# Optimization experiments

Hardware: AMD Instinct MI355X
Metric: run time of the kernel (lower is better)

Reference implementation:

```python
import jax, jax.numpy as jnp
import numpy as np

RADIUS = 50
HEADS = 4
BN_EPS = 1e-5


def setup_inputs() -> dict:
    key = jax.random.key(0)
    B, C, L = 2, 256, 1536
    D = C // HEADS
    ks = jax.random.split(key, 8)
    s = 0.05  # weight init scale
    return {
        "x": jax.random.normal(ks[0], (B, C, L), jnp.float32),
        "Wc": jax.random.normal(ks[1], (C, C), jnp.float32) * s,
        "bc": jnp.zeros((C,), jnp.float32),
        "Wq": jax.random.normal(ks[2], (C, C), jnp.float32) * s,
        "bq": jnp.zeros((C,), jnp.float32),
        "Wk": jax.random.normal(ks[3], (C, C), jnp.float32) * s,
        "bk": jnp.zeros((C,), jnp.float32),
        "emb": jax.random.normal(ks[4], (2 * RADIUS + 1, D), jnp.float32) * s,
        "Wf": jax.random.normal(ks[5], (C, C), jnp.float32) * s,
        "bf": jnp.zeros((C,), jnp.float32),
        "gamma": jnp.ones((C,), jnp.float32),
        "beta": jnp.zeros((C,), jnp.float32),
        "scale": jnp.full((C,), 0.1, jnp.float32),
    }


def reference(x, Wc, bc, Wq, bq, Wk, bk, emb, Wf, bf, gamma, beta, scale):
    B, C, L = x.shape
    H = HEADS
    D = C // H
    R = RADIUS

    def conv1x1(W, b, y):  # 1x1 Conv1d == per-position matmul
        return jnp.einsum('oc,bcl->bol', W, y) + b[None, :, None]

    def split(y):  # [B,C,L] -> [B,H,D,L]
        return y.reshape(B, H, D, L)

    content = split(conv1x1(Wc, bc, x))
    query = split(conv1x1(Wq, bq, x))
    key_ = split(conv1x1(Wk, bk, x))

    steps = jnp.arange(L)
    relative = steps[:, None] - steps[None, :]                 # [L,L]
    rel_clamped = jnp.clip(relative, -R, R)
    embs = emb[R + rel_clamped]                                # [L,L,D] gather

    dots = jnp.einsum('bhct,bhcs->bhts', query, key_)          # [B,H,L,L]
    dots = dots + 0.3 * jnp.einsum('bhct,tsc->bhts', query, embs)
    dots = jnp.where(jnp.abs(relative) <= R, dots, -jnp.inf)   # band mask

    weights = jax.nn.softmax(dots, axis=-1)                    # [B,H,L,L]

    out = jnp.einsum('bhts,bhcs->bhct', weights, content)      # [B,H,D,L]
    out = out + 0.3 * jnp.einsum('bhts,tsc->bhct', weights, embs)
    out = out.reshape(B, C, L)

    out = conv1x1(Wf, bf, out)
    # BatchNorm1d in training mode: batch stats over (B, L) per channel
    mean = out.mean(axis=(0, 2), keepdims=True)
    var = out.var(axis=(0, 2), keepdims=True)
    out = (out - mean) / jnp.sqrt(var + BN_EPS)
    out = out * gamma[None, :, None] + beta[None, :, None]
    return jax.nn.relu(out) * scale[None, :, None]
```

## Files before the change

### kernel.cpp

```cpp
#include <hip/hip_runtime.h>

typedef unsigned short u16;
typedef unsigned int u32;
typedef __bf16 bf16x8 __attribute__((ext_vector_type(8)));
typedef float f32x4 __attribute__((ext_vector_type(4)));

#define MFMA16 __builtin_amdgcn_mfma_f32_16x16x32_bf16

__device__ __forceinline__ u16 f2bf(float f) {
    u32 u = __float_as_uint(f);
    u32 r = (u + 0x7fffu + ((u >> 16) & 1u)) >> 16;
    return (u16)r;
}
__device__ __forceinline__ float bf2f(u16 h) {
    return __uint_as_float(((u32)h) << 16);
}
__device__ __forceinline__ bf16x8 ld8(const u16* p) {
    return *reinterpret_cast<const bf16x8*>(p);
}

__global__ __launch_bounds__(256) void prep_x(const float* __restrict__ x,
                                              u16* __restrict__ xT)
{
    __shared__ u16 tile[64][65];
    const int tid = threadIdx.x;
    const int b = blockIdx.z, c0 = blockIdx.y * 64, l0 = blockIdx.x * 64;
    const int cc = tid >> 2, lq = (tid & 3) * 16;
    const float* xp = x + (size_t)((b * 256 + c0 + cc) * 1536 + l0 + lq);
    #pragma unroll
    for (int i = 0; i < 4; ++i) {
        float4 v = *reinterpret_cast<const float4*>(xp + i * 4);
        tile[cc][lq + i * 4 + 0] = f2bf(v.x);
        tile[cc][lq + i * 4 + 1] = f2bf(v.y);
        tile[cc][lq + i * 4 + 2] = f2bf(v.z);
        tile[cc][lq + i * 4 + 3] = f2bf(v.w);
    }
    __syncthreads();
    const int ll = tid >> 2, cq = (tid & 3) * 16;
    u16* op = xT + (size_t)((b * 1536 + l0 + ll) * 256 + c0 + cq);
    #pragma unroll
    for (int i = 0; i < 16; ++i) op[i] = tile[cq + i][ll];
}

__global__ __launch_bounds__(256) void prep_we(
    const float* __restrict__ Wc, const float* __restrict__ Wq,
    const float* __restrict__ Wk, const float* __restrict__ Wf,
    const float* __restrict__ emb,
    u16* __restrict__ wcb, u16* __restrict__ wqb, u16* __restrict__ wkb,
    u16* __restrict__ wfb, u16* __restrict__ embR, u16* __restrict__ embT)
{
    const int i = blockIdx.x * 256 + threadIdx.x;
    if (i < 65536) {
        wcb[i] = f2bf(Wc[i]); wqb[i] = f2bf(Wq[i]);
        wkb[i] = f2bf(Wk[i]); wfb[i] = f2bf(Wf[i]);
    }
    if (i < 112 * 64) {
        int j = i >> 6, d = i & 63;
        embR[i] = (j < 101) ? f2bf(0.3f * emb[(100 - j) * 64 + d]) : (u16)0;
    }
    if (i < 64 * 128) {
        int d = i >> 7, j = i & 127;
        embT[i] = (j < 101) ? f2bf(0.3f * emb[(100 - j) * 64 + d]) : (u16)0;
    }
}

__global__ __launch_bounds__(256) void gemm_qk(
    const u16* __restrict__ xT,
    const u16* __restrict__ Wq, const float* __restrict__ bq,
    const u16* __restrict__ Wk, const float* __restrict__ bk,
    u16* __restrict__ qo, u16* __restrict__ ko)
{
    const int tid = threadIdx.x, wv = tid >> 6, lane = tid & 63;
    const int l15 = lane & 15, kg8 = (lane >> 4) * 8;
    const int z = blockIdx.z, b = z & 1, which = z >> 1;
    const u16* W = which ? Wk : Wq;
    const float* bias = which ? bk : bq;
    u16* outp = which ? ko : qo;
    const int m0 = blockIdx.x * 64 + (wv & 1) * 32;
    const int ch0 = blockIdx.y * 64 + (wv >> 1) * 32;
    const u16* ap = xT + (size_t)(b * 1536 + m0 + l15) * 256 + kg8;
    const u16* bp = W + (size_t)(ch0 + l15) * 256 + kg8;
    const f32x4 zf = {0.f, 0.f, 0.f, 0.f};
    f32x4 acc[2][2] = {{zf, zf}, {zf, zf}};
    #pragma unroll
    for (int kd = 0; kd < 8; ++kd) {
        bf16x8 a0 = ld8(ap + kd * 32);
        bf16x8 a1 = ld8(ap + 4096 + kd * 32);
        bf16x8 b0 = ld8(bp + kd * 32);
        bf16x8 b1 = ld8(bp + 4096 + kd * 32);
        acc[0][0] = MFMA16(a0, b0, acc[0][0], 0, 0, 0);
        acc[0][1] = MFMA16(a0, b1, acc[0][1], 0, 0, 0);
        acc[1][0] = MFMA16(a1, b0, acc[1][0], 0, 0, 0);
        acc[1][1] = MFMA16(a1, b1, acc[1][1], 0, 0, 0);
    }
    float bv[2];
    bv[0] = bias[ch0 + l15];
    bv[1] = bias[ch0 + 16 + l15];
    #pragma unroll
    for (int mf = 0; mf < 2; ++mf)
        #pragma unroll
        for (int nf = 0; nf < 2; ++nf)
            #pragma unroll
            for (int r = 0; r < 4; ++r) {
                const int row = m0 + mf * 16 + (lane >> 4) * 4 + r;
                outp[(size_t)(b * 1536 + row) * 256 + ch0 + nf * 16 + l15] =
                    f2bf(acc[mf][nf][r] + bv[nf]);
            }
}

__global__ __launch_bounds__(256) void gemm_cf(
    const u16* __restrict__ W, const float* __restrict__ bias,
    const u16* __restrict__ srcT, u16* __restrict__ outp)
{
    const int tid = threadIdx.x, wv = tid >> 6, lane = tid & 63;
    const int l15 = lane & 15, kg8 = (lane >> 4) * 8;
    const int b = blockIdx.z;
    const int l0 = blockIdx.x * 64 + (wv & 1) * 32;
    const int ch0 = blockIdx.y * 64 + (wv >> 1) * 32;
    const u16* ap = W + (size_t)(ch0 + l15) * 256 + kg8;
    const u16* bp = srcT + (size_t)(b * 1536 + l0 + l15) * 256 + kg8;
    const f32x4 zf = {0.f, 0.f, 0.f, 0.f};
    f32x4 acc[2][2] = {{zf, zf}, {zf, zf}};
    #pragma unroll
    for (int kd = 0; kd < 8; ++kd) {
        bf16x8 a0 = ld8(ap + kd * 32);
        bf16x8 a1 = ld8(ap + 4096 + kd * 32);
        bf16x8 b0 = ld8(bp + kd * 32);
        bf16x8 b1 = ld8(bp + 4096 + kd * 32);
        acc[0][0] = MFMA16(a0, b0, acc[0][0], 0, 0, 0);
        acc[0][1] = MFMA16(a0, b1, acc[0][1], 0, 0, 0);
        acc[1][0] = MFMA16(a1, b0, acc[1][0], 0, 0, 0);
        acc[1][1] = MFMA16(a1, b1, acc[1][1], 0, 0, 0);
    }
    #pragma unroll
    for (int mf = 0; mf < 2; ++mf)
        #pragma unroll
        for (int r = 0; r < 4; ++r) {
            const int ch = ch0 + mf * 16 + (lane >> 4) * 4 + r;
            const float bv = bias[ch];
            #pragma unroll
            for (int nf = 0; nf < 2; ++nf)
                outp[(size_t)(b * 256 + ch) * 1536 + l0 + nf * 16 + l15] =
                    f2bf(acc[mf][nf][r] + bv);
        }
}

#define WST 168
#define WBST 136
#define BST 114

__global__ __launch_bounds__(128) void attn_mfma(
    const u16* __restrict__ q, const u16* __restrict__ k,
    const u16* __restrict__ cont, const u16* __restrict__ embR,
    const u16* __restrict__ embT, u16* __restrict__ outp)
{
    __shared__ u16 wls[2][16][WST];
    __shared__ u16 wbs[2][16][WBST];
    __shared__ u16 bss[2][16][BST];
    const int tid = threadIdx.x;
    const int wv = tid >> 6, lane = tid & 63;
    const int l15 = lane & 15, kg8 = (lane >> 4) * 8;
    const int tt0 = (blockIdx.x * 2 + wv) * 16;
    const int bh = blockIdx.y, b = bh >> 2, h = bh & 3;
    u16* wl = &wls[wv][0][0];
    u16* wb = &wbs[wv][0][0];
    u16* bs = &bss[wv][0][0];

    for (int i = lane; i < 16 * 8; i += 64) {
        const int t = i >> 3, c = 144 + ((i & 7) << 1);
        *reinterpret_cast<u32*>(&wl[t * WST + c]) = 0;
    }
    for (int i = lane; i < 16 * 27; i += 64) {
        const int t = i / 27, j = 101 + (i - t * 27);
        wb[t * WBST + j] = 0;
    }

    const u16* qp = q + (size_t)(b * 1536 + tt0 + l15) * 256 + h * 64 + kg8;
    const bf16x8 a0 = ld8(qp);
    const bf16x8 a1 = ld8(qp + 32);
    const f32x4 zf = {0.f, 0.f, 0.f, 0.f};
    f32x4 dacc[9];
    f32x4 eacc[7];
    #pragma unroll
    for (int i = 0; i < 9; ++i) dacc[i] = zf;
    #pragma unroll
    for (int i = 0; i < 7; ++i) eacc[i] = zf;

    #pragma unroll
    for (int nf = 0; nf < 9; ++nf) {
        int s = tt0 - 64 + nf * 16 + l15;
        int sc = s < 0 ? 0 : (s > 1535 ? 1535 : s);
        const u16* kp = k + (size_t)(b * 1536 + sc) * 256 + h * 64 + kg8;
        dacc[nf] = MFMA16(a0, ld8(kp), dacc[nf], 0, 0, 0);
        dacc[nf] = MFMA16(a1, ld8(kp + 32), dacc[nf], 0, 0, 0);
    }
    #pragma unroll
    for (int jf = 0; jf < 7; ++jf) {
        const u16* ep = embR + (jf * 16 + l15) * 64 + kg8;
        eacc[jf] = MFMA16(a0, ld8(ep), eacc[jf], 0, 0, 0);
        eacc[jf] = MFMA16(a1, ld8(ep + 32), eacc[jf], 0, 0, 0);
    }
    #pragma unroll
    for (int jf = 0; jf < 7; ++jf)
        #pragma unroll
        for (int r = 0; r < 4; ++r) {
            const int t = (lane >> 4) * 4 + r;
            bs[t * BST + jf * 16 + l15] = f2bf(eacc[jf][r]);
        }
    #pragma unroll
    for (int nf = 0; nf < 9; ++nf)
        #pragma unroll
        for (int r = 0; r < 4; ++r) {
            const int t = (lane >> 4) * 4 + r;
            const int cs = nf * 16 + l15;
            const int j = cs - t - 14;
            const int s = tt0 - 64 + cs;
            float v = dacc[nf][r];
            if (j >= 0 && j < 101 && s >= 0 && s < 1536)
                v += bf2f(bs[t * BST + j]);
            else
                v = -1e30f;
            dacc[nf][r] = v;
        }
    float inv[4];
    #pragma unroll
    for (int r = 0; r < 4; ++r) {
        float m = dacc[0][r];
        #pragma unroll
        for (int nf = 1; nf < 9; ++nf) m = fmaxf(m, dacc[nf][r]);
        m = fmaxf(m, __shfl_xor(m, 1));
        m = fmaxf(m, __shfl_xor(m, 2));
        m = fmaxf(m, __shfl_xor(m, 4));
        m = fmaxf(m, __shfl_xor(m, 8));
        float ss = 0.f;
        #pragma unroll
        for (int nf = 0; nf < 9; ++nf) {
            float e = __expf(dacc[nf][r] - m);
            dacc[nf][r] = e;
            ss += e;
        }
        ss += __shfl_xor(ss, 1);
        ss += __shfl_xor(ss, 2);
        ss += __shfl_xor(ss, 4);
        ss += __shfl_xor(ss, 8);
        inv[r] = 1.f / ss;
    }
    #pragma unroll
    for (int nf = 0; nf < 9; ++nf)
        #pragma unroll
        for (int r = 0; r < 4; ++r) {
            const int t = (lane >> 4) * 4 + r;
            const int cs = nf * 16 + l15;
            const u16 w16 = f2bf(dacc[nf][r] * inv[r]);
            wl[t * WST + cs] = w16;
            const int j = cs - t - 14;
            if (j >= 0 && j < 101) wb[t * WBST + j] = w16;
        }

    f32x4 oacc[4];
    #pragma unroll
    for (int i = 0; i < 4; ++i) oacc[i] = zf;
    #pragma unroll
    for (int kf = 0; kf < 5; ++kf) {
        const bf16x8 aw = ld8(&wl[l15 * WST + kf * 32 + kg8]);
        int sb = tt0 - 64 + kf * 32 + kg8;
        int sbc = sb < 0 ? 0 : (sb > 1528 ? 1528 : sb);
        #pragma unroll
        for (int nf = 0; nf < 4; ++nf) {
            const u16* cp = cont + (size_t)(b * 256 + h * 64 + nf * 16 + l15) * 1536 + sbc;
            oacc[nf] = MFMA16(aw, ld8(cp), oacc[nf], 0, 0, 0);
        }
    }
    #pragma unroll
    for (int kf = 0; kf < 4; ++kf) {
        const bf16x8 ab = ld8(&wb[l15 * WBST + kf * 32 + kg8]);
        #pragma unroll
        for (int nf = 0; nf < 4; ++nf) {
            const u16* ep = embT + (nf * 16 + l15) * 128 + kf * 32 + kg8;
            oacc[nf] = MFMA16(ab, ld8(ep), oacc[nf], 0, 0, 0);
        }
    }
    #pragma unroll
    for (int nf = 0; nf < 4; ++nf)
        #pragma unroll
        for (int r = 0; r < 4; ++r) {
            const int t = (lane >> 4) * 4 + r;
            outp[(size_t)(b * 1536 + tt0 + t) * 256 + h * 64 + nf * 16 + l15] =
                f2bf(oacc[nf][r]);
        }
}

__global__ __launch_bounds__(256) void bn_apply(
    const u16* __restrict__ pre, const float* __restrict__ gamma,
    const float* __restrict__ beta, const float* __restrict__ scale,
    float* __restrict__ out)
{
    const int o = blockIdx.x;
    const int tid = threadIdx.x;
    float v[12];
    float sum = 0.f, sumsq = 0.f;
    #pragma unroll
    for (int i = 0; i < 12; ++i) {
        const int b = (i >= 6);
        const int l = (i - 6 * b) * 256 + tid;
        v[i] = bf2f(pre[(size_t)(b * 256 + o) * 1536 + l]);
        sum += v[i];
        sumsq = fmaf(v[i], v[i], sumsq);
    }
    #pragma unroll
    for (int off = 1; off < 64; off <<= 1) {
        sum += __shfl_xor(sum, off);
        sumsq += __shfl_xor(sumsq, off);
    }
    __shared__ float rs[4], rq[4];
    const int wave = tid >> 6;
    if ((tid & 63) == 0) { rs[wave] = sum; rq[wave] = sumsq; }
    __syncthreads();
    sum = rs[0] + rs[1] + rs[2] + rs[3];
    sumsq = rq[0] + rq[1] + rq[2] + rq[3];
    const float mean = sum * (1.f / 3072.f);
    const float var = sumsq * (1.f / 3072.f) - mean * mean;
    const float is = rsqrtf(var + 1e-5f);
    const float gm = gamma[o] * is;
    const float b2 = beta[o] - mean * gm;
    const float sc = scale[o];
    #pragma unroll
    for (int i = 0; i < 12; ++i) {
        const int b = (i >= 6);
        const int l = (i - 6 * b) * 256 + tid;
        out[(size_t)(b * 256 + o) * 1536 + l] = fmaxf(fmaf(v[i], gm, b2), 0.f) * sc;
    }
}

extern "C" void kernel_launch(void* const* d_in, const int* in_sizes, int n_in,
                              void* d_out, int out_size, void* d_ws, size_t ws_size,
                              hipStream_t stream) {
    const float* x     = (const float*)d_in[0];
    const float* Wc    = (const float*)d_in[1];
    const float* bc    = (const float*)d_in[2];
    const float* Wq    = (const float*)d_in[3];
    const float* bq    = (const float*)d_in[4];
    const float* Wk    = (const float*)d_in[5];
    const float* bk    = (const float*)d_in[6];
    const float* emb   = (const float*)d_in[7];
    const float* Wf    = (const float*)d_in[8];
    const float* bf    = (const float*)d_in[9];
    const float* gamma = (const float*)d_in[10];
    const float* beta  = (const float*)d_in[11];
    const float* scale = (const float*)d_in[12];
    float* out = (float*)d_out;
    u16* ws = (u16*)d_ws;

    const size_t NLC = 786432;
    u16* xT   = ws;
    u16* qb   = ws + NLC;
    u16* kb   = ws + 2 * NLC;
    u16* cbuf = ws + 3 * NLC;
    u16* abuf = ws + 4 * NLC;
    u16* pbuf = ws + 5 * NLC;
    u16* wcb  = ws + 6 * NLC;
    u16* wqb  = wcb + 65536;
    u16* wkb  = wqb + 65536;
    u16* wfb  = wkb + 65536;
    u16* embR = wfb + 65536;
    u16* embT = embR + 112 * 64;

    prep_x<<<dim3(24, 4, 2), 256, 0, stream>>>(x, xT);
    prep_we<<<256, 256, 0, stream>>>(Wc, Wq, Wk, Wf, emb, wcb, wqb, wkb, wfb, embR, embT);
    gemm_qk<<<dim3(24, 4, 4), 256, 0, stream>>>(xT, wqb, bq, wkb, bk, qb, kb);
    gemm_cf<<<dim3(24, 4, 2), 256, 0, stream>>>(wcb, bc, xT, cbuf);
    attn_mfma<<<dim3(48, 8), 128, 0, stream>>>(qb, kb, cbuf, embR, embT, abuf);
    gemm_cf<<<dim3(24, 4, 2), 256, 0, stream>>>(wfb, bf, abuf, pbuf);
    bn_apply<<<256, 256, 0, stream>>>(pbuf, gamma, beta, scale, out);
}
```

Baseline: 124.7 us.

## Merge prep kernels and Q/K/C projections into single launches with smaller blocks

Folds the x transpose and the weight/embedding conversion into one prep kernel keyed on blockIdx.z. The Q, K and content projections now run as one gemm_qkc launch. The projection and final GEMMs drop to 128-thread blocks with 32-channel tiles, doubling the grid so more blocks spread across the CUs. This cuts the launch count from seven to five and raises parallelism for the small GEMMs, at the cost of less reuse of the weight tile within each block.

```diff
diff --git a/kernel.cpp b/kernel.cpp
--- a/kernel.cpp
+++ b/kernel.cpp
@@ -19,67 +19,70 @@
     return *reinterpret_cast<const bf16x8*>(p);
 }
 
-__global__ __launch_bounds__(256) void prep_x(const float* __restrict__ x,
-                                              u16* __restrict__ xT)
-{
-    __shared__ u16 tile[64][65];
-    const int tid = threadIdx.x;
-    const int b = blockIdx.z, c0 = blockIdx.y * 64, l0 = blockIdx.x * 64;
-    const int cc = tid >> 2, lq = (tid & 3) * 16;
-    const float* xp = x + (size_t)((b * 256 + c0 + cc) * 1536 + l0 + lq);
-    #pragma unroll
-    for (int i = 0; i < 4; ++i) {
-        float4 v = *reinterpret_cast<const float4*>(xp + i * 4);
-        tile[cc][lq + i * 4 + 0] = f2bf(v.x);
-        tile[cc][lq + i * 4 + 1] = f2bf(v.y);
-        tile[cc][lq + i * 4 + 2] = f2bf(v.z);
-        tile[cc][lq + i * 4 + 3] = f2bf(v.w);
-    }
-    __syncthreads();
-    const int ll = tid >> 2, cq = (tid & 3) * 16;
-    u16* op = xT + (size_t)((b * 1536 + l0 + ll) * 256 + c0 + cq);
-    #pragma unroll
-    for (int i = 0; i < 16; ++i) op[i] = tile[cq + i][ll];
-}
-
-__global__ __launch_bounds__(256) void prep_we(
+__global__ __launch_bounds__(256) void prep(
+    const float* __restrict__ x,
     const float* __restrict__ Wc, const float* __restrict__ Wq,
     const float* __restrict__ Wk, const float* __restrict__ Wf,
     const float* __restrict__ emb,
+    u16* __restrict__ xT,
     u16* __restrict__ wcb, u16* __restrict__ wqb, u16* __restrict__ wkb,
     u16* __restrict__ wfb, u16* __restrict__ embR, u16* __restrict__ embT)
 {
-    const int i = blockIdx.x * 256 + threadIdx.x;
-    if (i < 65536) {
-        wcb[i] = f2bf(Wc[i]); wqb[i] = f2bf(Wq[i]);
-        wkb[i] = f2bf(Wk[i]); wfb[i] = f2bf(Wf[i]);
-    }
-    if (i < 112 * 64) {
-        int j = i >> 6, d = i & 63;
-        embR[i] = (j < 101) ? f2bf(0.3f * emb[(100 - j) * 64 + d]) : (u16)0;
-    }
-    if (i < 64 * 128) {
-        int d = i >> 7, j = i & 127;
-        embT[i] = (j < 101) ? f2bf(0.3f * emb[(100 - j) * 64 + d]) : (u16)0;
-    }
-}
-
-__global__ __launch_bounds__(256) void gemm_qk(
+    const int tid = threadIdx.x;
+    const int z = blockIdx.z;
+    if (z < 2) {
+        __shared__ u16 tile[64][65];
+        const int b = z, c0 = blockIdx.y * 64, l0 = blockIdx.x * 64;
+        const int cc = tid >> 2, lq = (tid & 3) * 16;
+        const float* xp = x + (size_t)((b * 256 + c0 + cc) * 1536 + l0 + lq);
+        #pragma unroll
+        for (int i = 0; i < 4; ++i) {
+            float4 v = *reinterpret_cast<const float4*>(xp + i * 4);
+            tile[cc][lq + i * 4 + 0] = f2bf(v.x);
+            tile[cc][lq + i * 4 + 1] = f2bf(v.y);
+            tile[cc][lq + i * 4 + 2] = f2bf(v.z);
+            tile[cc][lq + i * 4 + 3] = f2bf(v.w);
+        }
+        __syncthreads();
+        const int ll = tid >> 2, cq = (tid & 3) * 16;
+        u16* op = xT + (size_t)((b * 1536 + l0 + ll) * 256 + c0 + cq);
+        #pragma unroll
+        for (int i = 0; i < 16; ++i) op[i] = tile[cq + i][ll];
+    } else {
+        const int idx0 = (blockIdx.y * 24 + blockIdx.x) * 256 + tid;
+        for (int i = idx0; i < 65536; i += 24576) {
+            wcb[i] = f2bf(Wc[i]); wqb[i] = f2bf(Wq[i]);
+            wkb[i] = f2bf(Wk[i]); wfb[i] = f2bf(Wf[i]);
+        }
+        if (idx0 < 112 * 64) {
+            const int j = idx0 >> 6, d = idx0 & 63;
+            embR[idx0] = (j < 101) ? f2bf(0.3f * emb[(100 - j) * 64 + d]) : (u16)0;
+        }
+        if (idx0 < 64 * 128) {
+            const int d = idx0 >> 7, j = idx0 & 127;
+            embT[idx0] = (j < 101) ? f2bf(0.3f * emb[(100 - j) * 64 + d]) : (u16)0;
+        }
+    }
+}
+
+__global__ __launch_bounds__(128) void gemm_qkc(
     const u16* __restrict__ xT,
     const u16* __restrict__ Wq, const float* __restrict__ bq,
     const u16* __restrict__ Wk, const float* __restrict__ bk,
-    u16* __restrict__ qo, u16* __restrict__ ko)
+    const u16* __restrict__ Wc, const float* __restrict__ bc,
+    u16* __restrict__ qo, u16* __restrict__ ko, u16* __restrict__ co)
 {
     const int tid = threadIdx.x, wv = tid >> 6, lane = tid & 63;
     const int l15 = lane & 15, kg8 = (lane >> 4) * 8;
     const int z = blockIdx.z, b = z & 1, which = z >> 1;
-    const u16* W = which ? Wk : Wq;
-    const float* bias = which ? bk : bq;
-    u16* outp = which ? ko : qo;
-    const int m0 = blockIdx.x * 64 + (wv & 1) * 32;
-    const int ch0 = blockIdx.y * 64 + (wv >> 1) * 32;
-    const u16* ap = xT + (size_t)(b * 1536 + m0 + l15) * 256 + kg8;
-    const u16* bp = W + (size_t)(ch0 + l15) * 256 + kg8;
+    const u16* W = (which == 0) ? Wq : (which == 1) ? Wk : Wc;
+    const float* bias = (which == 0) ? bq : (which == 1) ? bk : bc;
+    const int l0 = blockIdx.x * 64 + wv * 32;
+    const int ch0 = blockIdx.y * 32;
+    const u16* xp = xT + (size_t)(b * 1536 + l0 + l15) * 256 + kg8;
+    const u16* wp = W + (size_t)(ch0 + l15) * 256 + kg8;
+    const u16* ap = (which == 2) ? wp : xp;
+    const u16* bp = (which == 2) ? xp : wp;
     const f32x4 zf = {0.f, 0.f, 0.f, 0.f};
     f32x4 acc[2][2] = {{zf, zf}, {zf, zf}};
     #pragma unroll
@@ -93,30 +96,45 @@
         acc[1][0] = MFMA16(a1, b0, acc[1][0], 0, 0, 0);
         acc[1][1] = MFMA16(a1, b1, acc[1][1], 0, 0, 0);
     }
-    float bv[2];
-    bv[0] = bias[ch0 + l15];
-    bv[1] = bias[ch0 + 16 + l15];
-    #pragma unroll
-    for (int mf = 0; mf < 2; ++mf)
-        #pragma unroll
-        for (int nf = 0; nf < 2; ++nf)
+    if (which < 2) {
+        u16* outp = which ? ko : qo;
+        float bv[2];
+        bv[0] = bias[ch0 + l15];
+        bv[1] = bias[ch0 + 16 + l15];
+        #pragma unroll
+        for (int mf = 0; mf < 2; ++mf)
+            #pragma unroll
+            for (int nf = 0; nf < 2; ++nf)
+                #pragma unroll
+                for (int r = 0; r < 4; ++r) {
+                    const int row = l0 + mf * 16 + (lane >> 4) * 4 + r;
+                    outp[(size_t)(b * 1536 + row) * 256 + ch0 + nf * 16 + l15] =
+                        f2bf(acc[mf][nf][r] + bv[nf]);
+                }
+    } else {
+        #pragma unroll
+        for (int mf = 0; mf < 2; ++mf)
             #pragma unroll
             for (int r = 0; r < 4; ++r) {
-                const int row = m0 + mf * 16 + (lane >> 4) * 4 + r;
-                outp[(size_t)(b * 1536 + row) * 256 + ch0 + nf * 16 + l15] =
-                    f2bf(acc[mf][nf][r] + bv[nf]);
+                const int ch = ch0 + mf * 16 + (lane >> 4) * 4 + r;
+                const float bv = bias[ch];
+                #pragma unroll
+                for (int nf = 0; nf < 2; ++nf)
+                    co[(size_t)(b * 256 + ch) * 1536 + l0 + nf * 16 + l15] =
+                        f2bf(acc[mf][nf][r] + bv);
             }
-}
-
-__global__ __launch_bounds__(256) void gemm_cf(
+    }
+}
+
+__global__ __launch_bounds__(128) void gemm_f(
     const u16* __restrict__ W, const float* __restrict__ bias,
     const u16* __restrict__ srcT, u16* __restrict__ outp)
 {
     const int tid = threadIdx.x, wv = tid >> 6, lane = tid & 63;
     const int l15 = lane & 15, kg8 = (lane >> 4) * 8;
     const int b = blockIdx.z;
-    const int l0 = blockIdx.x * 64 + (wv & 1) * 32;
-    const int ch0 = blockIdx.y * 64 + (wv >> 1) * 32;
+    const int l0 = blockIdx.x * 64 + wv * 32;
+    const int ch0 = blockIdx.y * 32;
     const u16* ap = W + (size_t)(ch0 + l15) * 256 + kg8;
     const u16* bp = srcT + (size_t)(b * 1536 + l0 + l15) * 256 + kg8;
     const f32x4 zf = {0.f, 0.f, 0.f, 0.f};
@@ -365,11 +383,11 @@
     u16* embR = wfb + 65536;
     u16* embT = embR + 112 * 64;
 
-    prep_x<<<dim3(24, 4, 2), 256, 0, stream>>>(x, xT);
-    prep_we<<<256, 256, 0, stream>>>(Wc, Wq, Wk, Wf, emb, wcb, wqb, wkb, wfb, embR, embT);
-    gemm_qk<<<dim3(24, 4, 4), 256, 0, stream>>>(xT, wqb, bq, wkb, bk, qb, kb);
-    gemm_cf<<<dim3(24, 4, 2), 256, 0, stream>>>(wcb, bc, xT, cbuf);
+    prep<<<dim3(24, 4, 3), 256, 0, stream>>>(x, Wc, Wq, Wk, Wf, emb,
+                                             xT, wcb, wqb, wkb, wfb, embR, embT);
+    gemm_qkc<<<dim3(24, 8, 6), 128, 0, stream>>>(xT, wqb, bq, wkb, bk, wcb, bc,
+                                                 qb, kb, cbuf);
     attn_mfma<<<dim3(48, 8), 128, 0, stream>>>(qb, kb, cbuf, embR, embT, abuf);
-    gemm_cf<<<dim3(24, 4, 2), 256, 0, stream>>>(wfb, bf, abuf, pbuf);
+    gemm_f<<<dim3(24, 8, 2), 128, 0, stream>>>(wfb, bf, abuf, pbuf);
     bn_apply<<<256, 256, 0, stream>>>(pbuf, gamma, beta, scale, out);
 }
```

Result: faster. 117.9 us (-5.4%).
